# Kernel optimization log

Hardware: AMD Instinct MI355X
Metric: run time of the kernel (lower is better)

## Reference

```python
import jax, jax.numpy as jnp
import numpy as np

H = 4    # heads
D = 64   # embed_dim


def setup_inputs() -> dict:
    key = jax.random.key(0)
    ks = jax.random.split(key, 10)
    N, L = 128, 1024
    f = jnp.float32
    return {
        "seq_items": jax.random.normal(ks[0], (N, L, D), f),
        "target_items": jax.random.normal(ks[1], (N, D), f),
        "memory": jax.random.normal(ks[2], (N, D), f),
        # nn.Linear weights stored torch-style [out_features, in_features]
        "Wk": jax.random.normal(ks[3], (H * D, D), f) * 0.1,
        "Wq": jax.random.normal(ks[4], (H * D, D), f) * 0.1,
        "Wv": jax.random.normal(ks[5], (H * D, D), f) * 0.1,
        "Wu": jax.random.normal(ks[6], (D, H * D), f) * 0.1,
        "bu": jnp.zeros((D,), f),
        "W1": jax.random.normal(ks[7], (8, 4 * D), f) * 0.1,
        "b1": jnp.zeros((8,), f),
        "W2": jax.random.normal(ks[8], (1, 8), f) * 0.1,
        "b2": jnp.zeros((1,), f),
    }


def reference(seq_items, target_items, memory, Wk, Wq, Wv, Wu, bu, W1, b1, W2, b2):
    N, L, d = seq_items.shape
    # projections, split into heads: [N, L, H, D]
    e = (seq_items @ Wk.T).reshape(N, L, H, D)
    V = (seq_items @ Wv.T).reshape(N, L, H, D)
    v = (target_items @ Wq.T).reshape(N, 1, H, D)   # broadcast over L
    m = memory.reshape(N, 1, 1, D)                   # broadcast over L and heads
    # np.where(e_, 1, 0): 1 where nonzero
    mask = (e != 0).astype(e.dtype)
    a1 = (v - e) * mask
    a2 = (v * e) * mask
    a3 = (m - e) * mask
    a4 = (m * e) * mask
    alpha = jnp.concatenate([a1, a2, a3, a4], axis=-1)  # [N, L, H, 4D]
    # tiny MLP attention scorer: 4D -> 8 -> 1, sigmoid each
    hmid = jax.nn.sigmoid(alpha @ W1.T + b1)
    att = jax.nn.sigmoid(hmid @ W2.T + b2)              # [N, L, H, 1]
    out = jnp.einsum('nlhq,nlhd->nqhd', att, V).reshape(N, H * D)
    output = out @ Wu.T + bu                            # [N, D]
    return output, att
```

## Files before the change

### kernel.cpp

```cpp
#include <hip/hip_runtime.h>
#include <math.h>

#define NN 128
#define LL 1024
#define HH 4
#define DD 64
#define NCHUNK 8
#define CROWS 128

#define WS_ZT  0
#define WS_C   16384
#define WS_WTB 20480

typedef __attribute__((ext_vector_type(8))) short short8;
typedef __attribute__((ext_vector_type(4))) float f32x4;

__device__ __forceinline__ float sigm(float x) {
    return __builtin_amdgcn_rcpf(1.f + __expf(-x));
}

__device__ __forceinline__ unsigned short f2bf(float x) {
    union { float f; unsigned u; } v; v.f = x;
    unsigned r = v.u + 0x7FFFu + ((v.u >> 16) & 1u);
    return (unsigned short)(r >> 16);
}

__device__ __forceinline__ short8 pack_bf8(float4 a, float4 b) {
    short8 r;
    r[0] = (short)f2bf(a.x); r[1] = (short)f2bf(a.y);
    r[2] = (short)f2bf(a.z); r[3] = (short)f2bf(a.w);
    r[4] = (short)f2bf(b.x); r[5] = (short)f2bf(b.y);
    r[6] = (short)f2bf(b.z); r[7] = (short)f2bf(b.w);
    return r;
}

__global__ void __launch_bounds__(256) precompute_kernel(
    const float* __restrict__ target, const float* __restrict__ memv,
    const float* __restrict__ Wk, const float* __restrict__ Wq,
    const float* __restrict__ Wv, const float* __restrict__ Wu,
    const float* __restrict__ W1, const float* __restrict__ b1,
    const float* __restrict__ bu,
    unsigned short* __restrict__ Wtb, float* __restrict__ cvg,
    float* __restrict__ Zt, float* __restrict__ out)
{
    const int b = blockIdx.x;
    const int t = threadIdx.x;

    if (b < 32) {
        const int idx = b * 256 + t;
        out[idx] = bu[idx & 63];
        return;
    }
    if (b < 96) {
        const int q = b - 32;
        const int h = t >> 6, k = t & 63;
        float s = 0.f;
        #pragma unroll 8
        for (int d = 0; d < 64; ++d)
            s = fmaf(Wu[q * 256 + h * 64 + d], Wv[(h * 64 + d) * 64 + k], s);
        Zt[t * 64 + q] = s;
        return;
    }

    const int nh = b - 96;
    const int n = nh >> 2, h = nh & 3;

    __shared__ __align__(16) float tl[64];
    __shared__ __align__(16) float ml[64];
    __shared__ float vh[64];
    __shared__ float wh[64 * 8];
    __shared__ float cp[64];

    if (t < 64)       tl[t] = target[n * 64 + t];
    else if (t < 128) ml[t - 64] = memv[n * 64 + (t - 64)];
    __syncthreads();

    {
        const int d = t >> 2, kq = t & 3;
        const float4* wq4 = reinterpret_cast<const float4*>(Wq + (h * 64 + d) * 64 + kq * 16);
        const float4* tl4 = reinterpret_cast<const float4*>(tl + kq * 16);
        float s = 0.f;
        #pragma unroll
        for (int c = 0; c < 4; ++c) {
            const float4 a = wq4[c], bb = tl4[c];
            s = fmaf(a.x, bb.x, s); s = fmaf(a.y, bb.y, s);
            s = fmaf(a.z, bb.z, s); s = fmaf(a.w, bb.w, s);
        }
        s += __shfl_xor(s, 1);
        s += __shfl_xor(s, 2);
        if (kq == 0) vh[d] = s;
    }
    __syncthreads();

    {
        const int d = t & 63, jh = t >> 6;
        const float vv = vh[d], mm = ml[d];
        #pragma unroll
        for (int r = 0; r < 2; ++r) {
            const int j = jh + r * 4;
            float wv = -W1[j * 256 + d] - W1[j * 256 + 128 + d];
            wv = fmaf(W1[j * 256 + 64 + d], vv, wv);
            wv = fmaf(W1[j * 256 + 192 + d], mm, wv);
            wh[d * 8 + j] = wv;
        }
    }
    if (t < 64) {
        const int j = t >> 3, sl = t & 7;
        float s = 0.f;
        #pragma unroll
        for (int d8 = 0; d8 < 8; ++d8) {
            const int d = sl * 8 + d8;
            s = fmaf(W1[j * 256 + d], vh[d], s);
            s = fmaf(W1[j * 256 + 128 + d], ml[d], s);
        }
        cp[t] = s;
    }
    __syncthreads();
    if (t < 8) {
        float s = b1[t];
        #pragma unroll
        for (int sl = 0; sl < 8; ++sl) s += cp[t * 8 + sl];
        cvg[n * 32 + h * 8 + t] = s;
    }

    {
        const int k = t & 63, jp = t >> 6;
        float s0 = 0.f, s1 = 0.f;
        #pragma unroll 8
        for (int d = 0; d < 64; ++d) {
            const float wk = Wk[(h * 64 + d) * 64 + k];
            s0 = fmaf(wk, wh[d * 8 + jp], s0);
            s1 = fmaf(wk, wh[d * 8 + jp + 4], s1);
        }
        unsigned short* dst = Wtb + ((size_t)n * 32 + h * 8) * 64;
        dst[jp * 64 + k]       = f2bf(s0);
        dst[(jp + 4) * 64 + k] = f2bf(s1);
    }
}

__global__ void __launch_bounds__(256, 4) main_kernel(
    const float* __restrict__ seq, const unsigned short* __restrict__ Wtb,
    const float* __restrict__ cvg, const float* __restrict__ W2,
    const float* __restrict__ b2, const float* __restrict__ Zt,
    float* __restrict__ att_out, float* __restrict__ out)
{
    const int n = blockIdx.x >> 3;
    const int chunk = blockIdx.x & 7;
    const int l0 = chunk * CROWS;
    const int t = threadIdx.x;
    const int lane = t & 63;
    const int w = t >> 6;

    __shared__ __align__(16) short seq_bf[128 * 72];
    __shared__ __align__(16) short wt_lds[32 * 72];
    __shared__ float cvl[32];
    __shared__ __align__(16) float att_l[512];
    __shared__ __align__(16) float Tp_l[4][256];
    __shared__ float T_l[256];
    __shared__ float op[256];

    const float* sbase = seq + ((size_t)n * LL + l0) * 64;

    #pragma unroll
    for (int g = 0; g < 4; ++g) {
        const int p4 = g * 256 + t;
        const int l = p4 >> 3, seg = p4 & 7;
        const float* rp = sbase + l * 64 + seg * 8;
        const float4 a = *reinterpret_cast<const float4*>(rp);
        const float4 bb = *reinterpret_cast<const float4*>(rp + 4);
        *reinterpret_cast<short8*>(seq_bf + l * 72 + seg * 8) = pack_bf8(a, bb);
    }
    {
        const int row = t >> 3, seg = t & 7;
        const int4 wv = *reinterpret_cast<const int4*>(
            Wtb + ((size_t)n * 32 + row) * 64 + seg * 8);
        *reinterpret_cast<int4*>(wt_lds + row * 72 + seg * 8) = wv;
    }
    if (t < 32) cvl[t] = cvg[n * 32 + t];
    __syncthreads();

    const int rt = w & 1;
    const int ctbase = (w >> 1) * 4;
    const int g = lane >> 4;
    const int cidx = lane & 15;

    short8 afrag[2];
    #pragma unroll
    for (int ks = 0; ks < 2; ++ks)
        afrag[ks] = *reinterpret_cast<const short8*>(
            wt_lds + (rt * 16 + cidx) * 72 + ks * 32 + g * 8);

    f32x4 acc[4];
    #pragma unroll
    for (int ct = 0; ct < 4; ++ct)
        #pragma unroll
        for (int r = 0; r < 4; ++r)
            acc[ct][r] = cvl[rt * 16 + g * 4 + r];

    #pragma unroll
    for (int ct = 0; ct < 4; ++ct) {
        const int l = (ctbase + ct) * 16 + cidx;
        const short8 bf0 = *reinterpret_cast<const short8*>(seq_bf + l * 72 + g * 8);
        const short8 bf1 = *reinterpret_cast<const short8*>(seq_bf + l * 72 + 32 + g * 8);
        acc[ct] = __builtin_amdgcn_mfma_f32_16x16x32_bf16(afrag[0], bf0, acc[ct], 0, 0, 0);
        acc[ct] = __builtin_amdgcn_mfma_f32_16x16x32_bf16(afrag[1], bf1, acc[ct], 0, 0, 0);
    }

    {
        const float4 w2v = *reinterpret_cast<const float4*>(W2 + 4 * (g & 1));
        const float b2v = b2[0];
        #pragma unroll
        for (int ct = 0; ct < 4; ++ct) {
            float local = w2v.x * sigm(acc[ct][0]);
            local = fmaf(w2v.y, sigm(acc[ct][1]), local);
            local = fmaf(w2v.z, sigm(acc[ct][2]), local);
            local = fmaf(w2v.w, sigm(acc[ct][3]), local);
            local += __shfl_xor(local, 16);
            const float attv = sigm(b2v + local);
            if ((lane & 16) == 0) {
                const int l = (ctbase + ct) * 16 + cidx;
                const int h = 2 * rt + (g >> 1);
                att_l[l * 4 + h] = attv;
            }
        }
    }
    __syncthreads();

    {
        float* dst = att_out + ((size_t)n * LL + l0) * 4;
        dst[t] = att_l[t];
        dst[256 + t] = att_l[256 + t];
    }

    {
        float th0 = 0.f, th1 = 0.f, th2 = 0.f, th3 = 0.f;
        const float* sq = sbase + (w * 32) * 64 + lane;
        #pragma unroll 4
        for (int li = 0; li < 32; ++li) {
            const float s = sq[li * 64];
            const float4 a = *reinterpret_cast<const float4*>(att_l + (w * 32 + li) * 4);
            th0 = fmaf(a.x, s, th0); th1 = fmaf(a.y, s, th1);
            th2 = fmaf(a.z, s, th2); th3 = fmaf(a.w, s, th3);
        }
        Tp_l[w][0 * 64 + lane] = th0;
        Tp_l[w][1 * 64 + lane] = th1;
        Tp_l[w][2 * 64 + lane] = th2;
        Tp_l[w][3 * 64 + lane] = th3;
    }
    __syncthreads();

    T_l[t] = Tp_l[0][t] + Tp_l[1][t] + Tp_l[2][t] + Tp_l[3][t];
    __syncthreads();

    {
        const int q = t & 63, wq = t >> 6;
        float s = 0.f;
        #pragma unroll 8
        for (int i = 0; i < 64; ++i) {
            const int p = wq * 64 + i;
            s = fmaf(T_l[p], Zt[p * 64 + q], s);
        }
        op[t] = s;
    }
    __syncthreads();
    if (t < 64) {
        const float s = op[t] + op[64 + t] + op[128 + t] + op[192 + t];
        atomicAdd(out + n * 64 + t, s);
    }
}

extern "C" void kernel_launch(void* const* d_in, const int* in_sizes, int n_in,
                              void* d_out, int out_size, void* d_ws, size_t ws_size,
                              hipStream_t stream) {
    const float* seq    = (const float*)d_in[0];
    const float* target = (const float*)d_in[1];
    const float* memv   = (const float*)d_in[2];
    const float* Wk     = (const float*)d_in[3];
    const float* Wq     = (const float*)d_in[4];
    const float* Wv     = (const float*)d_in[5];
    const float* Wu     = (const float*)d_in[6];
    const float* bu     = (const float*)d_in[7];
    const float* W1     = (const float*)d_in[8];
    const float* b1     = (const float*)d_in[9];
    const float* W2     = (const float*)d_in[10];
    const float* b2     = (const float*)d_in[11];

    float* out = (float*)d_out;
    float* att = out + NN * DD;

    float* ws  = (float*)d_ws;
    float* Ztw = ws + WS_ZT;
    float* cvg = ws + WS_C;
    unsigned short* Wtb = (unsigned short*)(ws + WS_WTB);

    precompute_kernel<<<608, 256, 0, stream>>>(target, memv, Wk, Wq, Wv, Wu, W1, b1,
                                               bu, Wtb, cvg, Ztw, out);
    main_kernel<<<NN * NCHUNK, 256, 0, stream>>>(seq, Wtb, cvg, W2, b2, Ztw,
                                                 att, out);
}
```

Before: 22.31 us.

## Fuse precompute and main kernels into one 1024-thread block per batch row

Merges the weight-folding precompute and the attention/pooling kernel into a single launch where each 1024-thread block handles one batch row, looping over the sequence in four 256-row chunks. The projected W1·Wk matrix and bias stay in shared memory instead of going through a workspace. The Wu·Wv product is replaced by per-row Wv then Wu matvecs, which removes the atomic accumulation and output init. This drops a launch and global round-trips but uses only 128 blocks, leaving many compute units idle and serializing chunk processing within a block.

```diff
diff --git a/kernel.cpp b/kernel.cpp
--- a/kernel.cpp
+++ b/kernel.cpp
@@ -5,12 +5,6 @@
 #define LL 1024
 #define HH 4
 #define DD 64
-#define NCHUNK 8
-#define CROWS 128
-
-#define WS_ZT  0
-#define WS_C   16384
-#define WS_WTB 20480
 
 typedef __attribute__((ext_vector_type(8))) short short8;
 typedef __attribute__((ext_vector_type(4))) float f32x4;
@@ -34,153 +28,108 @@
     return r;
 }
 
-__global__ void __launch_bounds__(256) precompute_kernel(
-    const float* __restrict__ target, const float* __restrict__ memv,
-    const float* __restrict__ Wk, const float* __restrict__ Wq,
-    const float* __restrict__ Wv, const float* __restrict__ Wu,
+__global__ void __launch_bounds__(1024, 4) fused_kernel(
+    const float* __restrict__ seq, const float* __restrict__ target,
+    const float* __restrict__ memv, const float* __restrict__ Wk,
+    const float* __restrict__ Wq, const float* __restrict__ Wv,
+    const float* __restrict__ Wu, const float* __restrict__ bu,
     const float* __restrict__ W1, const float* __restrict__ b1,
-    const float* __restrict__ bu,
-    unsigned short* __restrict__ Wtb, float* __restrict__ cvg,
-    float* __restrict__ Zt, float* __restrict__ out)
+    const float* __restrict__ W2, const float* __restrict__ b2,
+    float* __restrict__ att_out, float* __restrict__ out)
 {
-    const int b = blockIdx.x;
+    const int n = blockIdx.x;
     const int t = threadIdx.x;
-
-    if (b < 32) {
-        const int idx = b * 256 + t;
-        out[idx] = bu[idx & 63];
-        return;
-    }
-    if (b < 96) {
-        const int q = b - 32;
-        const int h = t >> 6, k = t & 63;
-        float s = 0.f;
-        #pragma unroll 8
-        for (int d = 0; d < 64; ++d)
-            s = fmaf(Wu[q * 256 + h * 64 + d], Wv[(h * 64 + d) * 64 + k], s);
-        Zt[t * 64 + q] = s;
-        return;
-    }
-
-    const int nh = b - 96;
-    const int n = nh >> 2, h = nh & 3;
+    const int lane = t & 63;
+    const int w = t >> 6;
 
     __shared__ __align__(16) float tl[64];
     __shared__ __align__(16) float ml[64];
-    __shared__ float vh[64];
-    __shared__ float wh[64 * 8];
-    __shared__ float cp[64];
+    __shared__ float vh[4][64];
+    __shared__ float wh[4][512];
+    __shared__ float cp[4][64];
+    __shared__ float cvl[32];
+    __shared__ __align__(16) short wt_lds[32 * 72];
+    __shared__ __align__(16) short seq_bf[256 * 72];
+    __shared__ __align__(16) float att_l[1024];
+    __shared__ __align__(16) float Tp_l[16][256];
+    __shared__ float T_l[256];
+    __shared__ __align__(16) float U_l[256];
+    __shared__ float op[16 * 64];
+
+    const int gg = t >> 8;
+    const int tt = t & 255;
+    const int h = gg;
 
     if (t < 64)       tl[t] = target[n * 64 + t];
     else if (t < 128) ml[t - 64] = memv[n * 64 + (t - 64)];
     __syncthreads();
 
     {
-        const int d = t >> 2, kq = t & 3;
+        const int d = tt >> 2, kq = tt & 3;
         const float4* wq4 = reinterpret_cast<const float4*>(Wq + (h * 64 + d) * 64 + kq * 16);
         const float4* tl4 = reinterpret_cast<const float4*>(tl + kq * 16);
         float s = 0.f;
         #pragma unroll
-        for (int c = 0; c < 4; ++c) {
-            const float4 a = wq4[c], bb = tl4[c];
+        for (int cc = 0; cc < 4; ++cc) {
+            const float4 a = wq4[cc], bb = tl4[cc];
             s = fmaf(a.x, bb.x, s); s = fmaf(a.y, bb.y, s);
             s = fmaf(a.z, bb.z, s); s = fmaf(a.w, bb.w, s);
         }
         s += __shfl_xor(s, 1);
         s += __shfl_xor(s, 2);
-        if (kq == 0) vh[d] = s;
-    }
-    __syncthreads();
-
-    {
-        const int d = t & 63, jh = t >> 6;
-        const float vv = vh[d], mm = ml[d];
+        if (kq == 0) vh[h][d] = s;
+    }
+    __syncthreads();
+
+    {
+        const int d = tt & 63, jh = tt >> 6;
+        const float vv = vh[h][d], mm = ml[d];
         #pragma unroll
         for (int r = 0; r < 2; ++r) {
             const int j = jh + r * 4;
             float wv = -W1[j * 256 + d] - W1[j * 256 + 128 + d];
             wv = fmaf(W1[j * 256 + 64 + d], vv, wv);
             wv = fmaf(W1[j * 256 + 192 + d], mm, wv);
-            wh[d * 8 + j] = wv;
-        }
-    }
-    if (t < 64) {
-        const int j = t >> 3, sl = t & 7;
+            wh[h][d * 8 + j] = wv;
+        }
+    }
+    if (tt < 64) {
+        const int j = tt >> 3, sl = tt & 7;
         float s = 0.f;
         #pragma unroll
         for (int d8 = 0; d8 < 8; ++d8) {
             const int d = sl * 8 + d8;
-            s = fmaf(W1[j * 256 + d], vh[d], s);
+            s = fmaf(W1[j * 256 + d], vh[h][d], s);
             s = fmaf(W1[j * 256 + 128 + d], ml[d], s);
         }
-        cp[t] = s;
-    }
-    __syncthreads();
-    if (t < 8) {
-        float s = b1[t];
-        #pragma unroll
-        for (int sl = 0; sl < 8; ++sl) s += cp[t * 8 + sl];
-        cvg[n * 32 + h * 8 + t] = s;
-    }
-
-    {
-        const int k = t & 63, jp = t >> 6;
+        cp[h][tt] = s;
+    }
+    __syncthreads();
+    if (tt < 8) {
+        float s = b1[tt];
+        #pragma unroll
+        for (int sl = 0; sl < 8; ++sl) s += cp[h][tt * 8 + sl];
+        cvl[h * 8 + tt] = s;
+    }
+
+    {
+        const int k = tt & 63, jp = tt >> 6;
         float s0 = 0.f, s1 = 0.f;
         #pragma unroll 8
         for (int d = 0; d < 64; ++d) {
             const float wk = Wk[(h * 64 + d) * 64 + k];
-            s0 = fmaf(wk, wh[d * 8 + jp], s0);
-            s1 = fmaf(wk, wh[d * 8 + jp + 4], s1);
-        }
-        unsigned short* dst = Wtb + ((size_t)n * 32 + h * 8) * 64;
-        dst[jp * 64 + k]       = f2bf(s0);
-        dst[(jp + 4) * 64 + k] = f2bf(s1);
-    }
-}
-
-__global__ void __launch_bounds__(256, 4) main_kernel(
-    const float* __restrict__ seq, const unsigned short* __restrict__ Wtb,
-    const float* __restrict__ cvg, const float* __restrict__ W2,
-    const float* __restrict__ b2, const float* __restrict__ Zt,
-    float* __restrict__ att_out, float* __restrict__ out)
-{
-    const int n = blockIdx.x >> 3;
-    const int chunk = blockIdx.x & 7;
-    const int l0 = chunk * CROWS;
-    const int t = threadIdx.x;
-    const int lane = t & 63;
-    const int w = t >> 6;
-
-    __shared__ __align__(16) short seq_bf[128 * 72];
-    __shared__ __align__(16) short wt_lds[32 * 72];
-    __shared__ float cvl[32];
-    __shared__ __align__(16) float att_l[512];
-    __shared__ __align__(16) float Tp_l[4][256];
-    __shared__ float T_l[256];
-    __shared__ float op[256];
-
-    const float* sbase = seq + ((size_t)n * LL + l0) * 64;
-
-    #pragma unroll
-    for (int g = 0; g < 4; ++g) {
-        const int p4 = g * 256 + t;
-        const int l = p4 >> 3, seg = p4 & 7;
-        const float* rp = sbase + l * 64 + seg * 8;
-        const float4 a = *reinterpret_cast<const float4*>(rp);
-        const float4 bb = *reinterpret_cast<const float4*>(rp + 4);
-        *reinterpret_cast<short8*>(seq_bf + l * 72 + seg * 8) = pack_bf8(a, bb);
-    }
-    {
-        const int row = t >> 3, seg = t & 7;
-        const int4 wv = *reinterpret_cast<const int4*>(
-            Wtb + ((size_t)n * 32 + row) * 64 + seg * 8);
-        *reinterpret_cast<int4*>(wt_lds + row * 72 + seg * 8) = wv;
-    }
-    if (t < 32) cvl[t] = cvg[n * 32 + t];
-    __syncthreads();
+            s0 = fmaf(wk, wh[h][d * 8 + jp], s0);
+            s1 = fmaf(wk, wh[h][d * 8 + jp + 4], s1);
+        }
+        wt_lds[(h * 8 + jp) * 72 + k]     = (short)f2bf(s0);
+        wt_lds[(h * 8 + jp + 4) * 72 + k] = (short)f2bf(s1);
+    }
+    __syncthreads();
+
+    const float* sbase = seq + (size_t)n * LL * 64;
 
     const int rt = w & 1;
-    const int ctbase = (w >> 1) * 4;
+    const int ctA = w >> 1;
     const int g = lane >> 4;
     const int cidx = lane & 15;
 
@@ -190,82 +139,118 @@
         afrag[ks] = *reinterpret_cast<const short8*>(
             wt_lds + (rt * 16 + cidx) * 72 + ks * 32 + g * 8);
 
-    f32x4 acc[4];
-    #pragma unroll
-    for (int ct = 0; ct < 4; ++ct)
-        #pragma unroll
-        for (int r = 0; r < 4; ++r)
-            acc[ct][r] = cvl[rt * 16 + g * 4 + r];
-
-    #pragma unroll
-    for (int ct = 0; ct < 4; ++ct) {
-        const int l = (ctbase + ct) * 16 + cidx;
-        const short8 bf0 = *reinterpret_cast<const short8*>(seq_bf + l * 72 + g * 8);
-        const short8 bf1 = *reinterpret_cast<const short8*>(seq_bf + l * 72 + 32 + g * 8);
-        acc[ct] = __builtin_amdgcn_mfma_f32_16x16x32_bf16(afrag[0], bf0, acc[ct], 0, 0, 0);
-        acc[ct] = __builtin_amdgcn_mfma_f32_16x16x32_bf16(afrag[1], bf1, acc[ct], 0, 0, 0);
-    }
-
-    {
-        const float4 w2v = *reinterpret_cast<const float4*>(W2 + 4 * (g & 1));
-        const float b2v = b2[0];
-        #pragma unroll
-        for (int ct = 0; ct < 4; ++ct) {
-            float local = w2v.x * sigm(acc[ct][0]);
-            local = fmaf(w2v.y, sigm(acc[ct][1]), local);
-            local = fmaf(w2v.z, sigm(acc[ct][2]), local);
-            local = fmaf(w2v.w, sigm(acc[ct][3]), local);
+    const float4 w2v = *reinterpret_cast<const float4*>(W2 + 4 * (g & 1));
+    const float b2v = b2[0];
+    const float cv0 = cvl[rt * 16 + g * 4 + 0];
+    const float cv1 = cvl[rt * 16 + g * 4 + 1];
+    const float cv2 = cvl[rt * 16 + g * 4 + 2];
+    const float cv3 = cvl[rt * 16 + g * 4 + 3];
+
+    float th0 = 0.f, th1 = 0.f, th2 = 0.f, th3 = 0.f;
+
+    for (int sc = 0; sc < 4; ++sc) {
+        const float* scb = sbase + sc * 256 * 64;
+
+        #pragma unroll
+        for (int gsg = 0; gsg < 2; ++gsg) {
+            const int p8 = gsg * 1024 + t;
+            const int l = p8 >> 3, seg = p8 & 7;
+            const float* rp = scb + l * 64 + seg * 8;
+            const float4 a = *reinterpret_cast<const float4*>(rp);
+            const float4 bb = *reinterpret_cast<const float4*>(rp + 4);
+            *reinterpret_cast<short8*>(seq_bf + l * 72 + seg * 8) = pack_bf8(a, bb);
+        }
+        __syncthreads();
+
+        #pragma unroll
+        for (int cc = 0; cc < 2; ++cc) {
+            const int ct = ctA + cc * 8;
+            const int l = ct * 16 + cidx;
+            f32x4 acc;
+            acc[0] = cv0; acc[1] = cv1; acc[2] = cv2; acc[3] = cv3;
+            const short8 bf0 = *reinterpret_cast<const short8*>(seq_bf + l * 72 + g * 8);
+            const short8 bf1 = *reinterpret_cast<const short8*>(seq_bf + l * 72 + 32 + g * 8);
+            acc = __builtin_amdgcn_mfma_f32_16x16x32_bf16(afrag[0], bf0, acc, 0, 0, 0);
+            acc = __builtin_amdgcn_mfma_f32_16x16x32_bf16(afrag[1], bf1, acc, 0, 0, 0);
+
+            float local = w2v.x * sigm(acc[0]);
+            local = fmaf(w2v.y, sigm(acc[1]), local);
+            local = fmaf(w2v.z, sigm(acc[2]), local);
+            local = fmaf(w2v.w, sigm(acc[3]), local);
             local += __shfl_xor(local, 16);
             const float attv = sigm(b2v + local);
             if ((lane & 16) == 0) {
-                const int l = (ctbase + ct) * 16 + cidx;
-                const int h = 2 * rt + (g >> 1);
-                att_l[l * 4 + h] = attv;
+                const int hh = 2 * rt + (g >> 1);
+                att_l[l * 4 + hh] = attv;
             }
         }
-    }
-    __syncthreads();
-
-    {
-        float* dst = att_out + ((size_t)n * LL + l0) * 4;
-        dst[t] = att_l[t];
-        dst[256 + t] = att_l[256 + t];
-    }
-
-    {
-        float th0 = 0.f, th1 = 0.f, th2 = 0.f, th3 = 0.f;
-        const float* sq = sbase + (w * 32) * 64 + lane;
-        #pragma unroll 4
-        for (int li = 0; li < 32; ++li) {
-            const float s = sq[li * 64];
-            const float4 a = *reinterpret_cast<const float4*>(att_l + (w * 32 + li) * 4);
-            th0 = fmaf(a.x, s, th0); th1 = fmaf(a.y, s, th1);
-            th2 = fmaf(a.z, s, th2); th3 = fmaf(a.w, s, th3);
-        }
-        Tp_l[w][0 * 64 + lane] = th0;
-        Tp_l[w][1 * 64 + lane] = th1;
-        Tp_l[w][2 * 64 + lane] = th2;
-        Tp_l[w][3 * 64 + lane] = th3;
-    }
-    __syncthreads();
-
-    T_l[t] = Tp_l[0][t] + Tp_l[1][t] + Tp_l[2][t] + Tp_l[3][t];
-    __syncthreads();
-
-    {
-        const int q = t & 63, wq = t >> 6;
-        float s = 0.f;
-        #pragma unroll 8
-        for (int i = 0; i < 64; ++i) {
-            const int p = wq * 64 + i;
-            s = fmaf(T_l[p], Zt[p * 64 + q], s);
-        }
-        op[t] = s;
+        __syncthreads();
+
+        att_out[((size_t)n * LL + sc * 256) * 4 + t] = att_l[t];
+
+        {
+            const float* sq = scb + (w * 16) * 64 + lane;
+            #pragma unroll 4
+            for (int li = 0; li < 16; ++li) {
+                const float s = sq[li * 64];
+                const float4 a = *reinterpret_cast<const float4*>(att_l + (w * 16 + li) * 4);
+                th0 = fmaf(a.x, s, th0); th1 = fmaf(a.y, s, th1);
+                th2 = fmaf(a.z, s, th2); th3 = fmaf(a.w, s, th3);
+            }
+        }
+    }
+
+    Tp_l[w][0 * 64 + lane] = th0;
+    Tp_l[w][1 * 64 + lane] = th1;
+    Tp_l[w][2 * 64 + lane] = th2;
+    Tp_l[w][3 * 64 + lane] = th3;
+    __syncthreads();
+
+    if (t < 256) {
+        float s = 0.f;
+        #pragma unroll
+        for (int i = 0; i < 16; ++i) s += Tp_l[i][t];
+        T_l[t] = s;
+    }
+    __syncthreads();
+
+    {
+        const int hd = t >> 2, kq = t & 3;
+        const int hq = hd >> 6;
+        const float4* wv4 = reinterpret_cast<const float4*>(Wv + hd * 64 + kq * 16);
+        const float4* t4  = reinterpret_cast<const float4*>(T_l + hq * 64 + kq * 16);
+        float s = 0.f;
+        #pragma unroll
+        for (int i = 0; i < 4; ++i) {
+            const float4 a = wv4[i], bb = t4[i];
+            s = fmaf(a.x, bb.x, s); s = fmaf(a.y, bb.y, s);
+            s = fmaf(a.z, bb.z, s); s = fmaf(a.w, bb.w, s);
+        }
+        s += __shfl_xor(s, 1);
+        s += __shfl_xor(s, 2);
+        if (kq == 0) U_l[hd] = s;
+    }
+    __syncthreads();
+
+    {
+        const int q = t & 63, qr = t >> 6;
+        const float4* wu4 = reinterpret_cast<const float4*>(Wu + q * 256 + qr * 16);
+        const float4* u4  = reinterpret_cast<const float4*>(U_l + qr * 16);
+        float s = 0.f;
+        #pragma unroll
+        for (int i = 0; i < 4; ++i) {
+            const float4 a = wu4[i], bb = u4[i];
+            s = fmaf(a.x, bb.x, s); s = fmaf(a.y, bb.y, s);
+            s = fmaf(a.z, bb.z, s); s = fmaf(a.w, bb.w, s);
+        }
+        op[qr * 64 + q] = s;
     }
     __syncthreads();
     if (t < 64) {
-        const float s = op[t] + op[64 + t] + op[128 + t] + op[192 + t];
-        atomicAdd(out + n * 64 + t, s);
+        float s = bu[t];
+        #pragma unroll
+        for (int qr = 0; qr < 16; ++qr) s += op[qr * 64 + t];
+        out[n * 64 + t] = s;
     }
 }
 
@@ -288,13 +273,6 @@
     float* out = (float*)d_out;
     float* att = out + NN * DD;
 
-    float* ws  = (float*)d_ws;
-    float* Ztw = ws + WS_ZT;
-    float* cvg = ws + WS_C;
-    unsigned short* Wtb = (unsigned short*)(ws + WS_WTB);
-
-    precompute_kernel<<<608, 256, 0, stream>>>(target, memv, Wk, Wq, Wv, Wu, W1, b1,
-                                               bu, Wtb, cvg, Ztw, out);
-    main_kernel<<<NN * NCHUNK, 256, 0, stream>>>(seq, Wtb, cvg, W2, b2, Ztw,
-                                                 att, out);
-}
+    fused_kernel<<<NN, 1024, 0, stream>>>(seq, target, memv, Wk, Wq, Wv, Wu,
+                                          bu, W1, b1, W2, b2, att, out);
+}
```

Measured after the change: 25.08 us. 1.12x slower.
